# Performance work log

Hardware: AMD Instinct MI355X
Metric: run time of the kernel (lower is better)

Reference implementation:

```python
import jax, jax.numpy as jnp
import numpy as np

B_, L_, D_, E_, N_, R_, K_ = 2, 2048, 2048, 4096, 16, 128, 4


def setup_inputs() -> dict:
    key = jax.random.key(0)
    ks = jax.random.split(key, 12)
    s = lambda k, shape, scale: jax.random.normal(k, shape, dtype=jnp.float32) * scale
    return {
        "resid": s(ks[0], (B_, L_, D_), 1.0),
        "norm_w": jnp.ones((D_,), jnp.float32),
        "W_skip": s(ks[1], (E_, D_), D_ ** -0.5),
        "W_in": s(ks[2], (E_, D_), D_ ** -0.5),
        "conv_w": s(ks[3], (E_, 1, K_), K_ ** -0.5),
        "conv_b": s(ks[4], (E_,), 0.02),
        "W_d1": s(ks[5], (R_, E_), E_ ** -0.5),
        "W_d2": s(ks[6], (E_, R_), R_ ** -0.5),
        "b_d2": s(ks[7], (E_,), 0.02) - 2.0,  # bias toward small delta like mamba dt init
        "W_Bm": s(ks[8], (N_, E_), E_ ** -0.5),
        "W_Cm": s(ks[9], (N_, E_), E_ ** -0.5),
        "A_log": s(ks[10], (E_, N_), 0.5),
        "W_D": jnp.ones((E_,), jnp.float32),
        "W_out": s(ks[11], (D_, E_), E_ ** -0.5),
    }


def reference(resid, norm_w, W_skip, W_in, conv_w, conv_b, W_d1, W_d2, b_d2,
              W_Bm, W_Cm, A_log, W_D, W_out):
    eps = 1e-5
    E, K = conv_w.shape[0], conv_w.shape[-1]
    # RMSNorm
    x = resid * jax.lax.rsqrt(jnp.mean(resid * resid, -1, keepdims=True) + eps) * norm_w
    skip = x @ W_skip.T                       # [B,L,E]
    x = x @ W_in.T                            # [B,L,E]
    # depthwise causal conv over L (torch pads both sides then cuts to L == left pad K-1)
    xc = jnp.swapaxes(x, 1, 2)                # [B,E,L]
    xc = jax.lax.conv_general_dilated(
        xc, conv_w, (1,), [(K - 1, 0)],
        dimension_numbers=("NCH", "OIH", "NCH"), feature_group_count=E)
    xc = xc + conv_b[None, :, None]
    x = jax.nn.silu(jnp.swapaxes(xc, 1, 2))   # [B,L,E] ssm input
    A = -jnp.exp(A_log)                       # [E,N]
    # input-dependent params, batched over B,L
    delta = jax.nn.softplus((x @ W_d1.T) @ W_d2.T + b_d2)  # [B,L,E]
    Bt = x @ W_Bm.T                           # [B,L,N]
    Ct = x @ W_Cm.T                           # [B,L,N]

    def step(h, inp):
        x_t, d_t, b_t, c_t = inp              # [B,E],[B,E],[B,N],[B,N]
        h = jnp.exp(d_t[:, :, None] * A) * h + (d_t * x_t)[:, :, None] * b_t[:, None, :]
        y = jnp.einsum("ben,bn->be", h, c_t)
        return h, y

    xs = (jnp.swapaxes(x, 0, 1), jnp.swapaxes(delta, 0, 1),
          jnp.swapaxes(Bt, 0, 1), jnp.swapaxes(Ct, 0, 1))
    h0 = jnp.zeros((x.shape[0], A.shape[0], A.shape[1]), x.dtype)
    _, ys = jax.lax.scan(step, h0, xs)        # [L,B,E]
    y = jnp.swapaxes(ys, 0, 1)                # [B,L,E]
    y = y + x * W_D
    y = y * jax.nn.silu(skip)
    return resid + y @ W_out.T
```

## Files before the change

### kernel.cpp

```cpp
#include <hip/hip_runtime.h>
#include <hip/hip_bf16.h>
#include <math.h>

#define MB_ 4096
#define DD_ 2048
#define EE_ 4096
#define LL_ 2048
#define NN_ 16
#define RR_ 128
#define CH_ 16
#define LCH_ (LL_ / CH_)

using short8  = __attribute__((ext_vector_type(8))) short;
using floatx4 = __attribute__((ext_vector_type(4))) float;
typedef unsigned short ushort_t;

__device__ __forceinline__ float bf2f(ushort_t u) {
    unsigned int x = ((unsigned int)u) << 16;
    return __builtin_bit_cast(float, x);
}
__device__ __forceinline__ ushort_t f2bf(float f) {
    unsigned int x = __builtin_bit_cast(unsigned int, f);
    unsigned int lsb = (x >> 16) & 1u;
    x += 0x7fffu + lsb;
    return (ushort_t)(x >> 16);
}
__device__ __forceinline__ float bf_lo(unsigned int u) {
    return __builtin_bit_cast(float, u << 16);
}
__device__ __forceinline__ float bf_hi(unsigned int u) {
    return __builtin_bit_cast(float, u & 0xffff0000u);
}

__device__ __forceinline__ void gld16(const ushort_t* g, ushort_t* l) {
    __builtin_amdgcn_global_load_lds(
        (const __attribute__((address_space(1))) unsigned int*)g,
        (__attribute__((address_space(3))) unsigned int*)l,
        16, 0, 0);
}

__global__ __launch_bounds__(256) void cvt_bf16_k(const float* __restrict__ src,
                                                  ushort_t* __restrict__ dst, int n4) {
    int i = blockIdx.x * 256 + threadIdx.x;
    if (i >= n4) return;
    float4 v = ((const float4*)src)[i];
    ushort_t* d = dst + (size_t)i * 4;
    d[0] = f2bf(v.x); d[1] = f2bf(v.y); d[2] = f2bf(v.z); d[3] = f2bf(v.w);
}

__global__ __launch_bounds__(256) void pack_bcd1_k(const float* __restrict__ Wb,
                                                   const float* __restrict__ Wc,
                                                   const float* __restrict__ Wd1,
                                                   ushort_t* __restrict__ dst) {
    int i = blockIdx.x * 256 + threadIdx.x;
    int row = i >> 10;
    int c4  = i & 1023;
    float4 v;
    if (row < 16)       v = ((const float4*)(Wb  + (size_t)row       * 4096))[c4];
    else if (row < 32)  v = ((const float4*)(Wc  + (size_t)(row - 16)* 4096))[c4];
    else if (row < 160) v = ((const float4*)(Wd1 + (size_t)(row - 32)* 4096))[c4];
    else { v.x = 0.f; v.y = 0.f; v.z = 0.f; v.w = 0.f; }
    ushort_t* d = dst + (size_t)i * 4;
    d[0] = f2bf(v.x); d[1] = f2bf(v.y); d[2] = f2bf(v.z); d[3] = f2bf(v.w);
}

__global__ __launch_bounds__(256) void rmsnorm_k(const float* __restrict__ resid,
                                                 const float* __restrict__ nw,
                                                 ushort_t* __restrict__ xn) {
    __shared__ float red[4];
    int row = blockIdx.x;
    int tid = threadIdx.x;
    const float* rp = resid + (size_t)row * DD_;
    float4 a = ((const float4*)rp)[tid];
    float4 b = ((const float4*)rp)[tid + 256];
    float ss = a.x*a.x + a.y*a.y + a.z*a.z + a.w*a.w
             + b.x*b.x + b.y*b.y + b.z*b.z + b.w*b.w;
    #pragma unroll
    for (int off = 32; off; off >>= 1) ss += __shfl_xor(ss, off);
    int wave = tid >> 6;
    if ((tid & 63) == 0) red[wave] = ss;
    __syncthreads();
    float total = red[0] + red[1] + red[2] + red[3];
    float scale = rsqrtf(total * (1.0f / (float)DD_) + 1e-5f);
    ushort_t* op = xn + (size_t)row * DD_;
    int i0 = tid * 4;
    op[i0+0] = f2bf(a.x * scale * nw[i0+0]);
    op[i0+1] = f2bf(a.y * scale * nw[i0+1]);
    op[i0+2] = f2bf(a.z * scale * nw[i0+2]);
    op[i0+3] = f2bf(a.w * scale * nw[i0+3]);
    int i1 = (tid + 256) * 4;
    op[i1+0] = f2bf(b.x * scale * nw[i1+0]);
    op[i1+1] = f2bf(b.y * scale * nw[i1+1]);
    op[i1+2] = f2bf(b.z * scale * nw[i1+2]);
    op[i1+3] = f2bf(b.w * scale * nw[i1+3]);
}

#define GMODE_BF16     0
#define GMODE_F32      1
#define GMODE_SOFTPLUS 2
#define GMODE_RESID    3

__global__ __launch_bounds__(256) void gemm_bt(
    const ushort_t* __restrict__ A, const ushort_t* __restrict__ Bw,
    int lda, int ldb, int K,
    void* __restrict__ outp, int ldc, int ncols,
    const float* __restrict__ aux, int mode)
{
    __shared__ __align__(16) ushort_t As[128 * 64];
    __shared__ __align__(16) ushort_t Bs[128 * 64];
    const int tid  = threadIdx.x;
    const int lane = tid & 63;
    const int wave = tid >> 6;
    const int quad = lane >> 4;
    const int l16  = lane & 15;
    const int mb   = (wave & 1) * 64;
    const int nb   = (wave >> 1) * 64;
    const int tileM = blockIdx.y * 128;
    const int tileN = blockIdx.x * 128;

    const int srow = wave * 8 + (lane >> 3);
    const int sq   = ((lane & 7) - (srow >> 1)) & 7;
    const ushort_t* Ag = A  + (size_t)(tileM + srow) * lda + sq * 8;
    const ushort_t* Bg = Bw + (size_t)(tileN + srow) * ldb + sq * 8;
    ushort_t* AsD = As + wave * 512;
    ushort_t* BsD = Bs + wave * 512;

    floatx4 acc[4][4];
    #pragma unroll
    for (int i = 0; i < 4; i++)
        #pragma unroll
        for (int j = 0; j < 4; j++)
            acc[i][j] = (floatx4){0.f, 0.f, 0.f, 0.f};

    int aoff[4][2], boff[4][2];
    #pragma unroll
    for (int i = 0; i < 4; i++) {
        int ar = mb + i * 16 + l16;
        int br = nb + i * 16 + l16;
        #pragma unroll
        for (int kk = 0; kk < 2; kk++) {
            aoff[i][kk] = ar * 64 + (((kk * 4 + quad) + (ar >> 1)) & 7) * 8;
            boff[i][kk] = br * 64 + (((kk * 4 + quad) + (br >> 1)) & 7) * 8;
        }
    }

    for (int kb = 0; kb < K; kb += 64) {
        __syncthreads();
        #pragma unroll
        for (int i = 0; i < 4; i++) {
            gld16(Ag + (size_t)i * 32 * lda + kb, AsD + i * 2048);
            gld16(Bg + (size_t)i * 32 * ldb + kb, BsD + i * 2048);
        }
        __syncthreads();
        #pragma unroll
        for (int kk = 0; kk < 2; kk++) {
            short8 af[4], bfr[4];
            #pragma unroll
            for (int i = 0; i < 4; i++)
                af[i] = *(const short8*)(As + aoff[i][kk]);
            #pragma unroll
            for (int j = 0; j < 4; j++)
                bfr[j] = *(const short8*)(Bs + boff[j][kk]);
            #pragma unroll
            for (int i = 0; i < 4; i++)
                #pragma unroll
                for (int j = 0; j < 4; j++)
                    acc[i][j] = __builtin_amdgcn_mfma_f32_16x16x32_bf16(af[i], bfr[j], acc[i][j], 0, 0, 0);
        }
    }

    #pragma unroll
    for (int i = 0; i < 4; i++) {
        #pragma unroll
        for (int j = 0; j < 4; j++) {
            int col = tileN + nb + j * 16 + l16;
            if (col >= ncols) continue;
            int rowb = tileM + mb + i * 16 + quad * 4;
            #pragma unroll
            for (int r = 0; r < 4; r++) {
                size_t idx = (size_t)(rowb + r) * ldc + col;
                float v = acc[i][j][r];
                if (mode == GMODE_BF16) {
                    ((ushort_t*)outp)[idx] = f2bf(v);
                } else if (mode == GMODE_F32) {
                    ((float*)outp)[idx] = v;
                } else if (mode == GMODE_SOFTPLUS) {
                    float z = v + aux[col];
                    float sp = (z > 20.f) ? z : log1pf(expf(z));
                    ((ushort_t*)outp)[idx] = f2bf(sp);
                } else {
                    ((float*)outp)[idx] = v + aux[idx];
                }
            }
        }
    }
}

__global__ __launch_bounds__(256) void conv_silu_k(const ushort_t* __restrict__ xin,
                                                   const float* __restrict__ cw,
                                                   const float* __restrict__ cb,
                                                   ushort_t* __restrict__ xs) {
    int e  = blockIdx.x * 256 + threadIdx.x;
    int l0 = blockIdx.y * 4;
    int b  = blockIdx.z;
    float w0 = cw[e * 4 + 0], w1 = cw[e * 4 + 1], w2 = cw[e * 4 + 2], w3 = cw[e * 4 + 3];
    float bias = cb[e];
    const ushort_t* p = xin + ((size_t)(b * LL_ + l0)) * EE_ + e;
    ushort_t*       o = xs  + ((size_t)(b * LL_ + l0)) * EE_ + e;
    float v[7];
    #pragma unroll
    for (int j = 0; j < 7; j++) {
        int l = l0 + j - 3;
        v[j] = (l >= 0) ? bf2f(p[(ptrdiff_t)(j - 3) * EE_]) : 0.f;
    }
    #pragma unroll
    for (int r = 0; r < 4; r++) {
        float s = bias + v[r] * w0 + v[r+1] * w1 + v[r+2] * w2 + v[r+3] * w3;
        float out = s / (1.f + expf(-s));
        o[(size_t)r * EE_] = f2bf(out);
    }
}

__global__ __launch_bounds__(256) void scan1_k(
    const ushort_t* __restrict__ xs, const ushort_t* __restrict__ delta,
    const ushort_t* __restrict__ bc, const float* __restrict__ A_log,
    float* __restrict__ P, float* __restrict__ S)
{
    const int e = blockIdx.x * 256 + threadIdx.x;
    const int c = blockIdx.y;
    const int b = blockIdx.z;
    const int l0 = c * LCH_;

    float acoef[NN_];
    {
        const float4* ap = (const float4*)(A_log + (size_t)e * NN_);
        #pragma unroll
        for (int k = 0; k < 4; k++) {
            float4 v = ap[k];
            acoef[k*4+0] = -expf(v.x) * 1.44269504f;
            acoef[k*4+1] = -expf(v.y) * 1.44269504f;
            acoef[k*4+2] = -expf(v.z) * 1.44269504f;
            acoef[k*4+3] = -expf(v.w) * 1.44269504f;
        }
    }

    const size_t m0 = (size_t)(b * LL_ + l0);
    const ushort_t* dp  = delta + m0 * EE_ + e;
    const ushort_t* xp  = xs    + m0 * EE_ + e;
    const ushort_t* bcp = bc    + m0 * 160;

    float h[NN_];
    #pragma unroll
    for (int n = 0; n < NN_; n++) h[n] = 0.f;
    float sd = 0.f;

    for (int l = 0; l < LCH_; ++l) {
        float dlt = bf2f(*dp); dp += EE_;
        float xv  = bf2f(*xp); xp += EE_;
        unsigned int q[4];
        *(uint4*)q = *(const uint4*)(bcp);
        unsigned int q2[4];
        *(uint4*)q2 = *(const uint4*)(bcp + 8);
        bcp += 160;
        sd += dlt;
        float dx = dlt * xv;
        float Bn[NN_];
        #pragma unroll
        for (int k = 0; k < 4; k++) {
            Bn[k*2+0] = bf_lo(q[k]);  Bn[k*2+1] = bf_hi(q[k]);
            Bn[8+k*2] = bf_lo(q2[k]); Bn[9+k*2] = bf_hi(q2[k]);
        }
        #pragma unroll
        for (int n = 0; n < NN_; n++) {
            float a = exp2f(dlt * acoef[n]);
            h[n] = fmaf(a, h[n], dx * Bn[n]);
        }
    }

    const size_t ob = (((size_t)(b * CH_ + c)) * EE_ + e) * NN_;
    float4* Pp = (float4*)(P + ob);
    float4* Sp = (float4*)(S + ob);
    #pragma unroll
    for (int k = 0; k < 4; k++) {
        float4 pv, sv;
        pv.x = exp2f(acoef[k*4+0] * sd); pv.y = exp2f(acoef[k*4+1] * sd);
        pv.z = exp2f(acoef[k*4+2] * sd); pv.w = exp2f(acoef[k*4+3] * sd);
        sv.x = h[k*4+0]; sv.y = h[k*4+1]; sv.z = h[k*4+2]; sv.w = h[k*4+3];
        Pp[k] = pv; Sp[k] = sv;
    }
}

__global__ __launch_bounds__(256) void scan2_k(const float* __restrict__ P, float* S) {
    int idx = blockIdx.x * 256 + threadIdx.x;
    int b  = idx >> 16;
    int en = idx & 65535;
    size_t base = ((size_t)b * CH_) * (EE_ * NN_) + en;
    float h = 0.f;
    #pragma unroll
    for (int c = 0; c < CH_; c++) {
        size_t o = base + (size_t)c * (EE_ * NN_);
        float Pv = P[o];
        float Sv = S[o];
        S[o] = h;
        h = fmaf(Pv, h, Sv);
    }
}

__global__ __launch_bounds__(256) void scan3_k(
    const ushort_t* __restrict__ xs, const ushort_t* delta,
    const ushort_t* __restrict__ bc, const ushort_t* __restrict__ skip,
    const float* __restrict__ A_log, const float* __restrict__ WD,
    const float* __restrict__ S, ushort_t* ys)
{
    const int e = blockIdx.x * 256 + threadIdx.x;
    const int c = blockIdx.y;
    const int b = blockIdx.z;
    const int l0 = c * LCH_;

    float acoef[NN_];
    {
        const float4* ap = (const float4*)(A_log + (size_t)e * NN_);
        #pragma unroll
        for (int k = 0; k < 4; k++) {
            float4 v = ap[k];
            acoef[k*4+0] = -expf(v.x) * 1.44269504f;
            acoef[k*4+1] = -expf(v.y) * 1.44269504f;
            acoef[k*4+2] = -expf(v.z) * 1.44269504f;
            acoef[k*4+3] = -expf(v.w) * 1.44269504f;
        }
    }
    const float wd = WD[e];

    float h[NN_];
    {
        const float4* Sp = (const float4*)(S + (((size_t)(b * CH_ + c)) * EE_ + e) * NN_);
        #pragma unroll
        for (int k = 0; k < 4; k++) {
            float4 v = Sp[k];
            h[k*4+0] = v.x; h[k*4+1] = v.y; h[k*4+2] = v.z; h[k*4+3] = v.w;
        }
    }

    const size_t m0 = (size_t)(b * LL_ + l0);
    const ushort_t* dp  = delta + m0 * EE_ + e;
    const ushort_t* xp  = xs    + m0 * EE_ + e;
    const ushort_t* sp  = skip  + m0 * EE_ + e;
    const ushort_t* bcp = bc    + m0 * 160;
    ushort_t*       yp  = ys    + m0 * EE_ + e;

    for (int l = 0; l < LCH_; ++l) {
        float dlt = bf2f(*dp); dp += EE_;
        float xv  = bf2f(*xp); xp += EE_;
        float sk  = bf2f(*sp); sp += EE_;
        unsigned int q[8];
        *(uint4*)(q)     = *(const uint4*)(bcp);
        *(uint4*)(q + 4) = *(const uint4*)(bcp + 8);
        unsigned int r[8];
        *(uint4*)(r)     = *(const uint4*)(bcp + 16);
        *(uint4*)(r + 4) = *(const uint4*)(bcp + 24);
        bcp += 160;
        float dx = dlt * xv;
        float y = 0.f;
        #pragma unroll
        for (int k = 0; k < 8; k++) {
            float B0 = bf_lo(q[k]), B1 = bf_hi(q[k]);
            float C0 = bf_lo(r[k]), C1 = bf_hi(r[k]);
            float a0 = exp2f(dlt * acoef[k*2+0]);
            float a1 = exp2f(dlt * acoef[k*2+1]);
            h[k*2+0] = fmaf(a0, h[k*2+0], dx * B0);
            h[k*2+1] = fmaf(a1, h[k*2+1], dx * B1);
            y = fmaf(h[k*2+0], C0, y);
            y = fmaf(h[k*2+1], C1, y);
        }
        y = (y + xv * wd) * (sk / (1.f + expf(-sk)));
        *yp = f2bf(y); yp += EE_;
    }
}

extern "C" void kernel_launch(void* const* d_in, const int* in_sizes, int n_in,
                              void* d_out, int out_size, void* d_ws, size_t ws_size,
                              hipStream_t stream) {
    const float* resid  = (const float*)d_in[0];
    const float* norm_w = (const float*)d_in[1];
    const float* W_skip = (const float*)d_in[2];
    const float* W_in   = (const float*)d_in[3];
    const float* conv_w = (const float*)d_in[4];
    const float* conv_b = (const float*)d_in[5];
    const float* W_d1   = (const float*)d_in[6];
    const float* W_d2   = (const float*)d_in[7];
    const float* b_d2   = (const float*)d_in[8];
    const float* W_Bm   = (const float*)d_in[9];
    const float* W_Cm   = (const float*)d_in[10];
    const float* A_log  = (const float*)d_in[11];
    const float* W_D    = (const float*)d_in[12];
    const float* W_out  = (const float*)d_in[13];
    float* out = (float*)d_out;

    const size_t MB16 = (size_t)16 * 1024 * 1024;
    const size_t MB32 = (size_t)32 * 1024 * 1024;
    char* w = (char*)d_ws;
    ushort_t* xn     = (ushort_t*)w;
    float*    Pbuf   = (float*)w;
    ushort_t* woutb  = (ushort_t*)w;
    w += MB16;
    ushort_t* wbuf   = (ushort_t*)w;
    ushort_t* wbcd1b = wbuf;
    ushort_t* wd2b   = wbuf + (size_t)256 * EE_;
    ushort_t* bcd1b  = wd2b + (size_t)EE_ * RR_;
    float*    Sbuf   = (float*)(bcd1b + (size_t)MB_ * 160);
    w += MB16;
    ushort_t* skipb  = (ushort_t*)w; w += MB32;
    ushort_t* xinb   = (ushort_t*)w;
    ushort_t* deltab = xinb;
    ushort_t* ysb    = xinb;
    w += MB32;
    ushort_t* xsb    = (ushort_t*)w; w += MB32;

    rmsnorm_k<<<MB_, 256, 0, stream>>>(resid, norm_w, xn);

    cvt_bf16_k<<<8192, 256, 0, stream>>>(W_skip, wbuf, (EE_ * DD_) / 4);
    gemm_bt<<<dim3(EE_ / 128, MB_ / 128), 256, 0, stream>>>(
        xn, wbuf, DD_, DD_, DD_, skipb, EE_, EE_, nullptr, GMODE_BF16);

    cvt_bf16_k<<<8192, 256, 0, stream>>>(W_in, wbuf, (EE_ * DD_) / 4);
    gemm_bt<<<dim3(EE_ / 128, MB_ / 128), 256, 0, stream>>>(
        xn, wbuf, DD_, DD_, DD_, xinb, EE_, EE_, nullptr, GMODE_BF16);

    pack_bcd1_k<<<1024, 256, 0, stream>>>(W_Bm, W_Cm, W_d1, wbcd1b);
    cvt_bf16_k<<<512, 256, 0, stream>>>(W_d2, wd2b, (EE_ * RR_) / 4);

    conv_silu_k<<<dim3(EE_ / 256, LL_ / 4, 2), 256, 0, stream>>>(xinb, conv_w, conv_b, xsb);

    gemm_bt<<<dim3(2, MB_ / 128), 256, 0, stream>>>(
        xsb, wbcd1b, EE_, EE_, EE_, bcd1b, 160, 160, nullptr, GMODE_BF16);

    gemm_bt<<<dim3(EE_ / 128, MB_ / 128), 256, 0, stream>>>(
        bcd1b + 32, wd2b, 160, RR_, RR_, deltab, EE_, EE_, b_d2, GMODE_SOFTPLUS);

    scan1_k<<<dim3(EE_ / 256, CH_, 2), 256, 0, stream>>>(
        xsb, deltab, bcd1b, A_log, Pbuf, Sbuf);
    scan2_k<<<(2 * EE_ * NN_) / 256, 256, 0, stream>>>(Pbuf, Sbuf);
    scan3_k<<<dim3(EE_ / 256, CH_, 2), 256, 0, stream>>>(
        xsb, deltab, bcd1b, skipb, A_log, W_D, Sbuf, ysb);

    cvt_bf16_k<<<8192, 256, 0, stream>>>(W_out, woutb, (DD_ * EE_) / 4);
    gemm_bt<<<dim3(DD_ / 128, MB_ / 128), 256, 0, stream>>>(
        ysb, woutb, EE_, EE_, EE_, out, DD_, DD_, resid, GMODE_RESID);
}
```

Baseline: 908.7 us.

## Add 256x256-tile 8-wave GEMM with staged prefetch for large projections

Adds a new bf16 MFMA GEMM kernel using 256x256 output tiles, 512 threads, a double-buffered LDS with swizzled layout, and a prefetch schedule that interleaves global-to-LDS loads with MFMA sub-blocks. It also remaps block IDs across groups of eight to improve L2 locality. The three big projection GEMMs (skip, in, out) switch to it, aiming to raise data reuse per tile and hide memory latency. The larger tile uses lots of LDS and registers, which lowers occupancy, and yields fewer blocks (e.g. 128 for the out projection) on a GPU with many CUs.

```diff
diff --git a/kernel.cpp b/kernel.cpp
--- a/kernel.cpp
+++ b/kernel.cpp
@@ -194,6 +194,177 @@
             }
         }
     }
+}
+
+__global__ __launch_bounds__(512) void gemm256(
+    const ushort_t* __restrict__ A, const ushort_t* __restrict__ Bw,
+    int lda, int ldb, int K,
+    void* __restrict__ outp, int ldc, int ncols,
+    const float* __restrict__ aux, int mode)
+{
+    __shared__ __align__(16) ushort_t lds[2][2][256 * 64];
+
+    const int tid  = threadIdx.x;
+    const int lane = tid & 63;
+    const int wave = tid >> 6;
+    const int wr   = wave >> 2;
+    const int wc   = wave & 3;
+    const int quad = lane >> 4;
+    const int l16  = lane & 15;
+    const int l8   = lane >> 3;
+    const int g8   = (lane & 7) ^ l8;
+
+    const int nx  = gridDim.x;
+    int bid = blockIdx.y * nx + blockIdx.x;
+    const int cpx = (nx * gridDim.y) >> 3;
+    bid = (bid & 7) * cpx + (bid >> 3);
+    const int tileM = (bid / nx) * 256;
+    const int tileN = (bid % nx) * 256;
+
+    const int arow = wr * 128 + wc * 8 + l8;
+    const int brow = wave * 8 + l8;
+    const ushort_t* Ag = A  + (size_t)(tileM + arow) * lda + g8 * 8;
+    const ushort_t* Bg = Bw + (size_t)(tileN + brow) * ldb + g8 * 8;
+    const int adst = (wr * 128 + wc * 8) * 64;
+    const int bdst = (wave * 8) * 64;
+
+#define STAGE_A(buf, t, r) gld16(Ag + (size_t)(r) * 32 * lda + (t) * 64, \
+                                 &lds[buf][0][adst + (r) * 32 * 64])
+#define STAGE_B(buf, t, r) gld16(Bg + (size_t)(r) * 64 * ldb + (t) * 64, \
+                                 &lds[buf][1][bdst + (r) * 64 * 64])
+
+    const int csw   = (quad ^ (l16 & 7)) * 8;
+    const int abase = (wr * 128 + l16) * 64 + csw;
+    const int bbase = (wc * 64 + l16) * 64 + csw;
+
+    floatx4 acc[4][2][4];
+    #pragma unroll
+    for (int mq = 0; mq < 4; mq++)
+        #pragma unroll
+        for (int mi = 0; mi < 2; mi++)
+            #pragma unroll
+            for (int n = 0; n < 4; n++)
+                acc[mq][mi][n] = (floatx4){0.f, 0.f, 0.f, 0.f};
+
+    short8 af[2][2];
+    short8 bfr[4][2];
+
+    const int NT = K >> 6;
+
+    #pragma unroll
+    for (int r = 0; r < 4; r++) STAGE_B(0, 0, r);
+    #pragma unroll
+    for (int r = 0; r < 4; r++) STAGE_A(0, 0, r);
+    if (NT > 1) {
+        #pragma unroll
+        for (int r = 0; r < 4; r++) STAGE_B(1, 1, r);
+        STAGE_A(1, 1, 0); STAGE_A(1, 1, 1);
+    }
+    asm volatile("s_waitcnt vmcnt(6)" ::: "memory");
+    __builtin_amdgcn_s_barrier();
+
+    for (int t = 0; t < NT; ++t) {
+        const int cur = t & 1;
+        const int nxt = cur ^ 1;
+        const bool s1 = (t + 1 < NT);
+        const bool s2 = (t + 2 < NT);
+
+        {
+            const ushort_t* Bb = lds[cur][1];
+            #pragma unroll
+            for (int n = 0; n < 4; n++) {
+                bfr[n][0] = *(const short8*)(Bb + (bbase + n * 1024));
+                bfr[n][1] = *(const short8*)(Bb + ((bbase ^ 32) + n * 1024));
+            }
+            const ushort_t* Ab = lds[cur][0];
+            #pragma unroll
+            for (int mi = 0; mi < 2; mi++) {
+                af[mi][0] = *(const short8*)(Ab + (abase + mi * 1024));
+                af[mi][1] = *(const short8*)(Ab + ((abase ^ 32) + mi * 1024));
+            }
+        }
+        if (s1) { STAGE_A(nxt, t + 1, 2); STAGE_A(nxt, t + 1, 3); }
+        __builtin_amdgcn_s_barrier();
+        asm volatile("s_waitcnt lgkmcnt(0)" ::: "memory");
+        __builtin_amdgcn_sched_barrier(0);
+        __builtin_amdgcn_s_setprio(1);
+        #pragma unroll
+        for (int kk = 0; kk < 2; kk++)
+            #pragma unroll
+            for (int mi = 0; mi < 2; mi++)
+                #pragma unroll
+                for (int n = 0; n < 4; n++)
+                    acc[0][mi][n] = __builtin_amdgcn_mfma_f32_16x16x32_bf16(
+                        af[mi][kk], bfr[n][kk], acc[0][mi][n], 0, 0, 0);
+        __builtin_amdgcn_s_setprio(0);
+        __builtin_amdgcn_s_barrier();
+
+        #pragma unroll
+        for (int mq = 1; mq < 4; mq++) {
+            {
+                const ushort_t* Ab = lds[cur][0];
+                #pragma unroll
+                for (int mi = 0; mi < 2; mi++) {
+                    af[mi][0] = *(const short8*)(Ab + (abase + mq * 2048 + mi * 1024));
+                    af[mi][1] = *(const short8*)(Ab + ((abase ^ 32) + mq * 2048 + mi * 1024));
+                }
+            }
+            if (s2) {
+                if (mq == 1) { STAGE_B(cur, t + 2, 0); STAGE_B(cur, t + 2, 1); }
+                if (mq == 2) { STAGE_B(cur, t + 2, 2); STAGE_B(cur, t + 2, 3); }
+                if (mq == 3) { STAGE_A(cur, t + 2, 0); STAGE_A(cur, t + 2, 1); }
+            }
+            __builtin_amdgcn_s_barrier();
+            asm volatile("s_waitcnt lgkmcnt(0)" ::: "memory");
+            __builtin_amdgcn_sched_barrier(0);
+            __builtin_amdgcn_s_setprio(1);
+            #pragma unroll
+            for (int kk = 0; kk < 2; kk++)
+                #pragma unroll
+                for (int mi = 0; mi < 2; mi++)
+                    #pragma unroll
+                    for (int n = 0; n < 4; n++)
+                        acc[mq][mi][n] = __builtin_amdgcn_mfma_f32_16x16x32_bf16(
+                            af[mi][kk], bfr[n][kk], acc[mq][mi][n], 0, 0, 0);
+            __builtin_amdgcn_s_setprio(0);
+            if (mq == 3) {
+                if (s2) asm volatile("s_waitcnt vmcnt(6)" ::: "memory");
+                else    asm volatile("s_waitcnt vmcnt(0)" ::: "memory");
+            }
+            __builtin_amdgcn_s_barrier();
+        }
+    }
+
+    #pragma unroll
+    for (int mq = 0; mq < 4; mq++) {
+        #pragma unroll
+        for (int mi = 0; mi < 2; mi++) {
+            #pragma unroll
+            for (int n = 0; n < 4; n++) {
+                int col = tileN + wc * 64 + n * 16 + l16;
+                if (col >= ncols) continue;
+                int rowb = tileM + wr * 128 + mq * 32 + mi * 16 + quad * 4;
+                #pragma unroll
+                for (int r = 0; r < 4; r++) {
+                    size_t idx = (size_t)(rowb + r) * ldc + col;
+                    float v = acc[mq][mi][n][r];
+                    if (mode == GMODE_BF16) {
+                        ((ushort_t*)outp)[idx] = f2bf(v);
+                    } else if (mode == GMODE_F32) {
+                        ((float*)outp)[idx] = v;
+                    } else if (mode == GMODE_SOFTPLUS) {
+                        float z = v + aux[col];
+                        float sp = (z > 20.f) ? z : log1pf(expf(z));
+                        ((ushort_t*)outp)[idx] = f2bf(sp);
+                    } else {
+                        ((float*)outp)[idx] = v + aux[idx];
+                    }
+                }
+            }
+        }
+    }
+#undef STAGE_A
+#undef STAGE_B
 }
 
 __global__ __launch_bounds__(256) void conv_silu_k(const ushort_t* __restrict__ xin,
@@ -419,11 +590,11 @@
     rmsnorm_k<<<MB_, 256, 0, stream>>>(resid, norm_w, xn);
 
     cvt_bf16_k<<<8192, 256, 0, stream>>>(W_skip, wbuf, (EE_ * DD_) / 4);
-    gemm_bt<<<dim3(EE_ / 128, MB_ / 128), 256, 0, stream>>>(
+    gemm256<<<dim3(EE_ / 256, MB_ / 256), 512, 0, stream>>>(
         xn, wbuf, DD_, DD_, DD_, skipb, EE_, EE_, nullptr, GMODE_BF16);
 
     cvt_bf16_k<<<8192, 256, 0, stream>>>(W_in, wbuf, (EE_ * DD_) / 4);
-    gemm_bt<<<dim3(EE_ / 128, MB_ / 128), 256, 0, stream>>>(
+    gemm256<<<dim3(EE_ / 256, MB_ / 256), 512, 0, stream>>>(
         xn, wbuf, DD_, DD_, DD_, xinb, EE_, EE_, nullptr, GMODE_BF16);
 
     pack_bcd1_k<<<1024, 256, 0, stream>>>(W_Bm, W_Cm, W_d1, wbcd1b);
@@ -444,6 +615,6 @@
         xsb, deltab, bcd1b, skipb, A_log, W_D, Sbuf, ysb);
 
     cvt_bf16_k<<<8192, 256, 0, stream>>>(W_out, woutb, (DD_ * EE_) / 4);
-    gemm_bt<<<dim3(DD_ / 128, MB_ / 128), 256, 0, stream>>>(
+    gemm256<<<dim3(DD_ / 256, MB_ / 256), 512, 0, stream>>>(
         ysb, woutb, EE_, EE_, EE_, out, DD_, DD_, resid, GMODE_RESID);
 }
```

Result: slower. 943.6 us (+3.8%).

## Add double-buffered LDS GEMM and use it for the three large projections

Applied to the files above, without the earlier changes.

Introduces gemm_db, a GEMM variant that keeps two LDS buffers for the A and B tiles and issues async global-to-LDS loads for the next K tile while MFMAs run on the current one, with a single barrier per iteration. It also reads fragments through inline ds_read_b128 with explicit waitcnt and a sched_barrier, so all LDS reads are issued before the MFMA block. The aim is to hide global load latency in the skip, in and out projections. The cost is double the shared memory (64 KB per block), which may reduce occupancy.

```diff
diff --git a/kernel.cpp b/kernel.cpp
--- a/kernel.cpp
+++ b/kernel.cpp
@@ -37,6 +37,13 @@
         (const __attribute__((address_space(1))) unsigned int*)g,
         (__attribute__((address_space(3))) unsigned int*)l,
         16, 0, 0);
+}
+
+typedef __attribute__((address_space(3))) const ushort_t* lds_cptr;
+__device__ __forceinline__ short8 dsr128(const ushort_t* p) {
+    short8 d;
+    asm volatile("ds_read_b128 %0, %1" : "=&v"(d) : "v"((lds_cptr)p));
+    return d;
 }
 
 __global__ __launch_bounds__(256) void cvt_bf16_k(const float* __restrict__ src,
@@ -167,6 +174,117 @@
                 for (int j = 0; j < 4; j++)
                     acc[i][j] = __builtin_amdgcn_mfma_f32_16x16x32_bf16(af[i], bfr[j], acc[i][j], 0, 0, 0);
         }
+    }
+
+    #pragma unroll
+    for (int i = 0; i < 4; i++) {
+        #pragma unroll
+        for (int j = 0; j < 4; j++) {
+            int col = tileN + nb + j * 16 + l16;
+            if (col >= ncols) continue;
+            int rowb = tileM + mb + i * 16 + quad * 4;
+            #pragma unroll
+            for (int r = 0; r < 4; r++) {
+                size_t idx = (size_t)(rowb + r) * ldc + col;
+                float v = acc[i][j][r];
+                if (mode == GMODE_BF16) {
+                    ((ushort_t*)outp)[idx] = f2bf(v);
+                } else if (mode == GMODE_F32) {
+                    ((float*)outp)[idx] = v;
+                } else if (mode == GMODE_SOFTPLUS) {
+                    float z = v + aux[col];
+                    float sp = (z > 20.f) ? z : log1pf(expf(z));
+                    ((ushort_t*)outp)[idx] = f2bf(sp);
+                } else {
+                    ((float*)outp)[idx] = v + aux[idx];
+                }
+            }
+        }
+    }
+}
+
+__global__ __launch_bounds__(256) void gemm_db(
+    const ushort_t* __restrict__ A, const ushort_t* __restrict__ Bw,
+    int lda, int ldb, int K,
+    void* __restrict__ outp, int ldc, int ncols,
+    const float* __restrict__ aux, int mode)
+{
+    __shared__ __align__(16) ushort_t As[2][128 * 64];
+    __shared__ __align__(16) ushort_t Bs[2][128 * 64];
+    const int tid  = threadIdx.x;
+    const int lane = tid & 63;
+    const int wave = tid >> 6;
+    const int quad = lane >> 4;
+    const int l16  = lane & 15;
+    const int mb   = (wave & 1) * 64;
+    const int nb   = (wave >> 1) * 64;
+    const int tileM = blockIdx.y * 128;
+    const int tileN = blockIdx.x * 128;
+
+    const int srow = wave * 8 + (lane >> 3);
+    const int sq   = ((lane & 7) - (srow >> 1)) & 7;
+    const ushort_t* Ag = A  + (size_t)(tileM + srow) * lda + sq * 8;
+    const ushort_t* Bg = Bw + (size_t)(tileN + srow) * ldb + sq * 8;
+    const int sdst = wave * 512;
+
+    floatx4 acc[4][4];
+    #pragma unroll
+    for (int i = 0; i < 4; i++)
+        #pragma unroll
+        for (int j = 0; j < 4; j++)
+            acc[i][j] = (floatx4){0.f, 0.f, 0.f, 0.f};
+
+    int aoff[4][2], boff[4][2];
+    #pragma unroll
+    for (int i = 0; i < 4; i++) {
+        int ar = mb + i * 16 + l16;
+        int br = nb + i * 16 + l16;
+        #pragma unroll
+        for (int kk = 0; kk < 2; kk++) {
+            aoff[i][kk] = ar * 64 + (((kk * 4 + quad) + (ar >> 1)) & 7) * 8;
+            boff[i][kk] = br * 64 + (((kk * 4 + quad) + (br >> 1)) & 7) * 8;
+        }
+    }
+
+    const int NT = K >> 6;
+
+    #pragma unroll
+    for (int i = 0; i < 4; i++) {
+        gld16(Ag + (size_t)i * 32 * lda, &As[0][sdst + i * 2048]);
+        gld16(Bg + (size_t)i * 32 * ldb, &Bs[0][sdst + i * 2048]);
+    }
+    asm volatile("s_waitcnt vmcnt(0)" ::: "memory");
+    __syncthreads();
+
+    for (int t = 0; t < NT; ++t) {
+        const int cur = t & 1;
+        if (t + 1 < NT) {
+            const int kb = (t + 1) << 6;
+            #pragma unroll
+            for (int i = 0; i < 4; i++) {
+                gld16(Ag + (size_t)i * 32 * lda + kb, &As[cur ^ 1][sdst + i * 2048]);
+                gld16(Bg + (size_t)i * 32 * ldb + kb, &Bs[cur ^ 1][sdst + i * 2048]);
+            }
+        }
+        #pragma unroll
+        for (int kk = 0; kk < 2; kk++) {
+            short8 af[4], bfr[4];
+            #pragma unroll
+            for (int i = 0; i < 4; i++)
+                af[i] = dsr128(&As[cur][aoff[i][kk]]);
+            #pragma unroll
+            for (int j = 0; j < 4; j++)
+                bfr[j] = dsr128(&Bs[cur][boff[j][kk]]);
+            asm volatile("s_waitcnt lgkmcnt(0)" ::: "memory");
+            __builtin_amdgcn_sched_barrier(0);
+            #pragma unroll
+            for (int i = 0; i < 4; i++)
+                #pragma unroll
+                for (int j = 0; j < 4; j++)
+                    acc[i][j] = __builtin_amdgcn_mfma_f32_16x16x32_bf16(af[i], bfr[j], acc[i][j], 0, 0, 0);
+        }
+        asm volatile("s_waitcnt vmcnt(0)" ::: "memory");
+        __syncthreads();
     }
 
     #pragma unroll
@@ -419,11 +537,11 @@
     rmsnorm_k<<<MB_, 256, 0, stream>>>(resid, norm_w, xn);
 
     cvt_bf16_k<<<8192, 256, 0, stream>>>(W_skip, wbuf, (EE_ * DD_) / 4);
-    gemm_bt<<<dim3(EE_ / 128, MB_ / 128), 256, 0, stream>>>(
+    gemm_db<<<dim3(EE_ / 128, MB_ / 128), 256, 0, stream>>>(
         xn, wbuf, DD_, DD_, DD_, skipb, EE_, EE_, nullptr, GMODE_BF16);
 
     cvt_bf16_k<<<8192, 256, 0, stream>>>(W_in, wbuf, (EE_ * DD_) / 4);
-    gemm_bt<<<dim3(EE_ / 128, MB_ / 128), 256, 0, stream>>>(
+    gemm_db<<<dim3(EE_ / 128, MB_ / 128), 256, 0, stream>>>(
         xn, wbuf, DD_, DD_, DD_, xinb, EE_, EE_, nullptr, GMODE_BF16);
 
     pack_bcd1_k<<<1024, 256, 0, stream>>>(W_Bm, W_Cm, W_d1, wbcd1b);
@@ -444,6 +562,6 @@
         xsb, deltab, bcd1b, skipb, A_log, W_D, Sbuf, ysb);
 
     cvt_bf16_k<<<8192, 256, 0, stream>>>(W_out, woutb, (DD_ * EE_) / 4);
-    gemm_bt<<<dim3(DD_ / 128, MB_ / 128), 256, 0, stream>>>(
+    gemm_db<<<dim3(DD_ / 128, MB_ / 128), 256, 0, stream>>>(
         ysb, woutb, EE_, EE_, EE_, out, DD_, DD_, resid, GMODE_RESID);
 }
```

Result: no change. 900.3 us (-0.9%).
